# Kernel tuning notes

Hardware: AMD Instinct MI355X
Metric: run time of the kernel (lower is better)

## Reference

```python
import jax, jax.numpy as jnp
import numpy as np
import math

B, C, H, W = 8, 256, 64, 64
KEYDIM, VALDIM = 128, 256


def conv3x3(x, w, b):
    # x: [B,C,H,W], w: [O,C,3,3] -> [B,O,H,W], SAME padding (padding=1)
    y = jax.lax.conv_general_dilated(x, w, window_strides=(1, 1), padding='SAME',
                                     dimension_numbers=('NCHW', 'OIHW', 'NCHW'))
    return y + b[None, :, None, None]


def setup_inputs() -> dict:
    key = jax.random.key(0)
    ks = jax.random.split(key, 5)
    x = jax.random.normal(ks[0], (B, C, H, W), dtype=jnp.float32)
    fan_in = C * 9
    s = 1.0 / np.sqrt(fan_in)
    key_w = jax.random.uniform(ks[1], (KEYDIM, C, 3, 3), jnp.float32, -s, s)
    key_b = jax.random.uniform(ks[2], (KEYDIM,), jnp.float32, -s, s)
    val_w = jax.random.uniform(ks[3], (VALDIM, C, 3, 3), jnp.float32, -s, s)
    val_b = jax.random.uniform(ks[4], (VALDIM,), jnp.float32, -s, s)
    return {"x": x, "key_w": key_w, "key_b": key_b, "val_w": val_w, "val_b": val_b}


def reference(x, key_w, key_b, val_w, val_b):
    b_, c_, h_, w_ = x.shape
    k = conv3x3(x, key_w, key_b).reshape(b_, KEYDIM, h_ * w_)   # [B,K,N]
    v = conv3x3(x, val_w, val_b)                                 # [B,V,H,W]
    sq = jnp.sum(k * k, axis=1)                                  # [B,N]
    a = sq[:, :, None]                                           # [B,N,1]
    c2 = sq[:, None, :]                                          # [B,1,N]
    dots = 2.0 * jnp.einsum('bki,bkj->bij', k, k)                # [B,N,N]
    affinity = (-a + dots - c2) / math.sqrt(KEYDIM)              # -||ki-kj||^2 / sqrt(K)
    affinity = jax.nn.softmax(affinity, axis=1)                  # softmax over dim=1 (rows)
    self_attn = jnp.einsum('bvi,bij->bvj', v.reshape(b_, VALDIM, h_ * w_), affinity)
    self_attn = self_attn.reshape(b_, VALDIM, h_, w_)
    return jnp.concatenate((v, self_attn), axis=1)               # [B,2V,H,W]
```

## Files before the change

### kernel.cpp

```cpp
#include <hip/hip_runtime.h>
#include <hip/hip_bf16.h>
#include <cstdint>

constexpr int Bb = 8, Cc = 256, Hh = 64, Ww = 64, Nn = 4096;
constexpr int KD = 128, VD = 256, HP = 66;

typedef __attribute__((ext_vector_type(8))) short short8_t;
typedef __attribute__((ext_vector_type(4))) short shortx4;
typedef __attribute__((ext_vector_type(4))) float floatx4;

constexpr float kScale = 0.08838834764831845f * 1.4426950408889634f;
constexpr float kTwoK  = 2.0f * kScale;

static __device__ __forceinline__ ushort f2bf(float f) {
    union { float f; uint32_t u; } v{f};
    uint32_t r = v.u + 0x7FFFu + ((v.u >> 16) & 1u);
    return (ushort)(r >> 16);
}
static __device__ __forceinline__ float bf2f(ushort b) {
    union { uint32_t u; float f; } v{(uint32_t)b << 16};
    return v.f;
}
static __device__ __forceinline__ uint32_t pk_bf16(float a, float b) {
    uint32_t r;
    asm("v_cvt_pk_bf16_f32 %0, %1, %2" : "=v"(r) : "v"(a), "v"(b));
    return r;
}
static __device__ __forceinline__ float exp2_raw(float x) {
    float r;
    asm("v_exp_f32 %0, %1" : "=v"(r) : "v"(x));
    return r;
}

static __device__ __forceinline__ void gload_lds16(const void* g, void* l) {
    __builtin_amdgcn_global_load_lds((const __attribute__((address_space(1))) uint32_t*)g,
                                     (__attribute__((address_space(3))) uint32_t*)l, 16, 0, 0);
}

__global__ __launch_bounds__(256) void pad_transpose(const float* __restrict__ x,
                                                     ushort* __restrict__ xpad) {
    int bid = blockIdx.x;
    int b = bid & 7, rest = bid >> 3;
    int y = rest & 63, cg = rest >> 6;
    int t = threadIdx.x;
    __shared__ float tile[64][65];
    int xcol = t & 63;
    int crow = t >> 6;
    const float* xb = x + ((size_t)(b * Cc + cg * 64) * Nn) + y * 64;
#pragma unroll
    for (int i = 0; i < 16; i++) {
        int c = crow + i * 4;
        tile[c][xcol] = xb[(size_t)c * Nn + xcol];
    }
    __syncthreads();
    int c = t & 63;
    int x4 = t >> 6;
    ushort* dst = xpad + (((size_t)(b * HP + (y + 1)) * HP) + 1) * Cc + cg * 64 + c;
#pragma unroll
    for (int i = 0; i < 16; i++) {
        int xx = x4 + i * 4;
        dst[(size_t)xx * Cc] = f2bf(tile[c][xx]);
    }
}

__global__ __launch_bounds__(256) void repack_w(const float* __restrict__ kw,
                                                const float* __restrict__ vw,
                                                ushort* __restrict__ wtk,
                                                ushort* __restrict__ wtv) {
    int idx = blockIdx.x * 256 + threadIdx.x;
    const int nk = KD * Cc;
    const int nv = VD * Cc;
    if (idx < nk) {
        const float* src = kw + (size_t)idx * 9;
        int oc = idx / Cc, c = idx % Cc;
#pragma unroll
        for (int r = 0; r < 9; r++) wtk[((size_t)r * KD + oc) * Cc + c] = f2bf(src[r]);
    } else if (idx < nk + nv) {
        int j = idx - nk;
        const float* src = vw + (size_t)j * 9;
        int oc = j / Cc, c = j % Cc;
#pragma unroll
        for (int r = 0; r < 9; r++) wtv[((size_t)r * VD + oc) * Cc + c] = f2bf(src[r]);
    }
}

__global__ __launch_bounds__(256) void conv_k(const ushort* __restrict__ xpad,
                                              const ushort* __restrict__ wt,
                                              const float* __restrict__ bias,
                                              ushort* __restrict__ kt_out,
                                              float* __restrict__ sq_out) {
    int bid = blockIdx.x;
    int b = bid & 7, y = bid >> 3;
    int lane = threadIdx.x & 63, wv = threadIdx.x >> 6;
    int l15 = lane & 15, g = lane >> 4;
    const int swzA = l15 & 7;

    __shared__ ushort wslab[2][128 * 128];

    size_t wsoff[8];
    int ldsrow[8];
#pragma unroll
    for (int h = 0; h < 8; h++) {
        int row = wv * 32 + h * 4 + (lane >> 4);
        wsoff[h] = (size_t)row * Cc + (((lane & 15) ^ (row & 7)) * 8);
        ldsrow[h] = (wv * 32 + h * 4) * 128;
    }

    floatx4 acc[8];
#pragma unroll
    for (int m = 0; m < 8; m++) acc[m] = (floatx4){0.f, 0.f, 0.f, 0.f};

    const ushort* xb = xpad + ((size_t)b * HP * HP) * Cc;
    int xcol = wv * 16 + l15;

    auto stage = [&](int hs, int bi) {
        int r = hs >> 1, hc = hs & 1;
        const ushort* wb = wt + ((size_t)r * KD) * Cc + hc * 128;
#pragma unroll
        for (int h = 0; h < 8; h++)
            gload_lds16(wb + wsoff[h], &wslab[bi][ldsrow[h]]);
    };

    stage(0, 0);
    __syncthreads();

#pragma unroll 1
    for (int hs = 0; hs < 18; ++hs) {
        int bi = hs & 1;
        if (hs < 17) stage(hs + 1, bi ^ 1);

        int r = hs >> 1, hc = hs & 1;
        int dy = r / 3, dx = r % 3;
        const ushort* bsrc = xb + ((size_t)(y + dy) * HP + xcol + dx) * Cc + hc * 128 + g * 8;
#pragma unroll
        for (int cc = 0; cc < 4; cc++) {
            short8_t bfrag = *(const short8_t*)(bsrc + cc * 32);
#pragma unroll
            for (int m = 0; m < 8; m++) {
                short8_t afrag = *(const short8_t*)&wslab[bi][(m * 16 + l15) * 128 + ((cc * 4 + g) ^ swzA) * 8];
                acc[m] = __builtin_amdgcn_mfma_f32_16x16x32_bf16(afrag, bfrag, acc[m], 0, 0, 0);
            }
        }
        __syncthreads();
    }

    int pos = y * 64 + xcol;
    ushort* kt = kt_out + ((size_t)(b * Nn + pos)) * KD;
    float ssum = 0.f;
#pragma unroll
    for (int m = 0; m < 8; m++) {
        floatx4 bv = *(const floatx4*)(bias + m * 16 + g * 4);
        shortx4 pk;
#pragma unroll
        for (int r = 0; r < 4; r++) {
            pk[r] = (short)f2bf(acc[m][r] + bv[r]);
            float q = bf2f((ushort)pk[r]);
            ssum += q * q;
        }
        *(shortx4*)(kt + m * 16 + g * 4) = pk;
    }
    ssum += __shfl_xor(ssum, 16, 64);
    ssum += __shfl_xor(ssum, 32, 64);
    if (g == 0) sq_out[b * Nn + pos] = ssum * kScale;
}

__global__ __launch_bounds__(256) void conv_v(const ushort* __restrict__ xpad,
                                              const ushort* __restrict__ wt,
                                              const float* __restrict__ bias,
                                              float* __restrict__ f32_out,
                                              ushort* __restrict__ vb_out) {
    int bid = blockIdx.x;
    int b = bid & 7;
    int ocg = (bid >> 3) & 1;
    int y0 = (bid >> 4) * 2;
    int lane = threadIdx.x & 63, wv = threadIdx.x >> 6;
    int l15 = lane & 15, g = lane >> 4;
    int oc0 = ocg * 128;
    const int swzA = l15 & 7;

    __shared__ ushort wslab[2][128 * 128];

    size_t wsoff[8];
    int ldsrow[8];
#pragma unroll
    for (int h = 0; h < 8; h++) {
        int row = wv * 32 + h * 4 + (lane >> 4);
        wsoff[h] = (size_t)row * Cc + (((lane & 15) ^ (row & 7)) * 8);
        ldsrow[h] = (wv * 32 + h * 4) * 128;
    }

    floatx4 acc[8][2];
#pragma unroll
    for (int m = 0; m < 8; m++)
#pragma unroll
        for (int rr = 0; rr < 2; rr++) acc[m][rr] = (floatx4){0.f, 0.f, 0.f, 0.f};

    const ushort* xb = xpad + ((size_t)b * HP * HP) * Cc;
    int xcol = wv * 16 + l15;

    auto stage = [&](int hs, int bi) {
        int r = hs >> 1, hc = hs & 1;
        const ushort* wb = wt + ((size_t)r * VD + oc0) * Cc + hc * 128;
#pragma unroll
        for (int h = 0; h < 8; h++)
            gload_lds16(wb + wsoff[h], &wslab[bi][ldsrow[h]]);
    };

    stage(0, 0);
    __syncthreads();

#pragma unroll 1
    for (int hs = 0; hs < 18; ++hs) {
        int bi = hs & 1;
        if (hs < 17) stage(hs + 1, bi ^ 1);

        int r = hs >> 1, hc = hs & 1;
        int dy = r / 3, dx = r % 3;
        const ushort* bsrc0 = xb + ((size_t)(y0 + dy) * HP + xcol + dx) * Cc + hc * 128 + g * 8;
        const ushort* bsrc1 = bsrc0 + (size_t)HP * Cc;
#pragma unroll
        for (int cc = 0; cc < 4; cc++) {
            short8_t bfragA = *(const short8_t*)(bsrc0 + cc * 32);
            short8_t bfragB = *(const short8_t*)(bsrc1 + cc * 32);
#pragma unroll
            for (int m = 0; m < 8; m++) {
                short8_t afrag = *(const short8_t*)&wslab[bi][(m * 16 + l15) * 128 + ((cc * 4 + g) ^ swzA) * 8];
                acc[m][0] = __builtin_amdgcn_mfma_f32_16x16x32_bf16(afrag, bfragA, acc[m][0], 0, 0, 0);
                acc[m][1] = __builtin_amdgcn_mfma_f32_16x16x32_bf16(afrag, bfragB, acc[m][1], 0, 0, 0);
            }
        }
        __syncthreads();
    }

#pragma unroll
    for (int rr = 0; rr < 2; rr++) {
        int pos = (y0 + rr) * 64 + xcol;
#pragma unroll
        for (int m = 0; m < 8; m++) {
            floatx4 bv = *(const floatx4*)(bias + oc0 + m * 16 + g * 4);
#pragma unroll
            for (int r = 0; r < 4; r++) {
                int oc = oc0 + m * 16 + g * 4 + r;
                float v = acc[m][rr][r] + bv[r];
                f32_out[((size_t)(b * 512 + oc)) * Nn + pos] = v;
                vb_out[((size_t)(b * VD + oc)) * Nn + pos] = f2bf(v);
            }
        }
    }
}

__global__ __launch_bounds__(256) void attn_kernel(const ushort* __restrict__ kt,
                                                   const ushort* __restrict__ vb,
                                                   const float* __restrict__ sq2,
                                                   float* __restrict__ out) {
    int bid = blockIdx.x;
    int b = bid & 7, jt = bid >> 3;
    int lane = threadIdx.x & 63, wv = threadIdx.x >> 6;
    int l15 = lane & 15, g = lane >> 4;

    __shared__ ushort bufK[64 * 128];
    __shared__ ushort bufV[256 * 64];
    __shared__ ushort pt[4][16][72];
    __shared__ float dls[4][16];

    const ushort* ktb = kt + ((size_t)b * Nn) * KD;
    const ushort* vbb = vb + ((size_t)b * VD) * Nn;
    const float* sqb = sq2 + b * Nn;

    const ushort* skp[4];
#pragma unroll
    for (int h = 0; h < 4; h++) {
        int row = wv * 16 + h * 4 + (lane >> 4);
        skp[h] = ktb + (size_t)row * KD + (((lane & 15) ^ (row & 7)) * 8);
    }
    const ushort* svp[8];
#pragma unroll
    for (int h = 0; h < 8; h++) {
        int vd = wv * 64 + h * 8 + (lane >> 3);
        svp[h] = vbb + (size_t)vd * Nn + (((lane & 7) ^ (vd & 7)) * 8);
    }

    int j = jt * 64 + wv * 16 + l15;
    short8_t kj[4];
#pragma unroll
    for (int kk = 0; kk < 4; kk++)
        kj[kk] = *(const short8_t*)(ktb + (size_t)j * KD + kk * 32 + g * 8);

    const int vh = wv >> 1, jh = wv & 1;

    floatx4 acc[8][2];
#pragma unroll
    for (int m = 0; m < 8; m++)
#pragma unroll
        for (int s = 0; s < 2; s++) acc[m][s] = (floatx4){0.f, 0.f, 0.f, 0.f};
    float dsum = 0.f;
    const int swzA = l15 & 7;

#pragma unroll
    for (int h = 0; h < 4; h++) gload_lds16(skp[h], &bufK[(wv * 16 + h * 4) * 128]);
#pragma unroll
    for (int h = 0; h < 8; h++) gload_lds16(svp[h], &bufV[(wv * 64 + h * 8) * 64]);
    __syncthreads();

#pragma unroll 1
    for (int it = 0; it < 64; ++it) {
        int i0 = it * 64;

        floatx4 sacc[4];
#pragma unroll
        for (int f = 0; f < 4; f++) sacc[f] = (floatx4){0.f, 0.f, 0.f, 0.f};
#pragma unroll
        for (int kk = 0; kk < 4; kk++) {
#pragma unroll
            for (int f = 0; f < 4; f++) {
                short8_t afr = *(const short8_t*)&bufK[(f * 16 + l15) * 128 + ((kk * 4 + g) ^ swzA) * 8];
                sacc[f] = __builtin_amdgcn_mfma_f32_16x16x32_bf16(afr, kj[kk], sacc[f], 0, 0, 0);
            }
        }
#pragma unroll
        for (int f = 0; f < 4; f++) {
            floatx4 sqi = *(const floatx4*)(sqb + i0 + f * 16 + g * 4);
            float p0 = exp2_raw(sacc[f][0] * kTwoK - sqi[0]);
            float p1 = exp2_raw(sacc[f][1] * kTwoK - sqi[1]);
            float p2 = exp2_raw(sacc[f][2] * kTwoK - sqi[2]);
            float p3 = exp2_raw(sacc[f][3] * kTwoK - sqi[3]);
            dsum += (p0 + p1) + (p2 + p3);
            uint2 w2 = {pk_bf16(p0, p1), pk_bf16(p2, p3)};
            *(uint2*)&pt[wv][l15][f * 16 + g * 4] = w2;
        }
        __syncthreads();

        if (it < 63) {
#pragma unroll
            for (int h = 0; h < 4; h++)
                gload_lds16(skp[h] + (size_t)(i0 + 64) * KD, &bufK[(wv * 16 + h * 4) * 128]);
        }

#pragma unroll
        for (int k2 = 0; k2 < 2; k2++) {
            short8_t pfr[2];
#pragma unroll
            for (int s = 0; s < 2; s++)
                pfr[s] = *(const short8_t*)&pt[jh * 2 + s][l15][k2 * 32 + g * 8];
#pragma unroll
            for (int m = 0; m < 8; m++) {
                int row = vh * 128 + m * 16 + l15;
                short8_t vfr = *(const short8_t*)&bufV[row * 64 + ((k2 * 4 + g) ^ swzA) * 8];
#pragma unroll
                for (int s = 0; s < 2; s++)
                    acc[m][s] = __builtin_amdgcn_mfma_f32_16x16x32_bf16(vfr, pfr[s], acc[m][s], 0, 0, 0);
            }
        }
        __syncthreads();

        if (it < 63) {
#pragma unroll
            for (int h = 0; h < 8; h++)
                gload_lds16(svp[h] + (i0 + 64), &bufV[(wv * 64 + h * 8) * 64]);
        }
    }

    dsum += __shfl_xor(dsum, 16, 64);
    dsum += __shfl_xor(dsum, 32, 64);
    if (g == 0) dls[wv][l15] = dsum;
    __syncthreads();
    float rden[2];
#pragma unroll
    for (int s = 0; s < 2; s++) rden[s] = 1.f / dls[jh * 2 + s][l15];

    float* ob = out + ((size_t)(b * 512 + 256 + vh * 128)) * Nn + jt * 64 + jh * 32 + l15;
#pragma unroll
    for (int m = 0; m < 8; m++) {
#pragma unroll
        for (int s = 0; s < 2; s++) {
#pragma unroll
            for (int r = 0; r < 4; r++) {
                int vd = m * 16 + g * 4 + r;
                ob[(size_t)vd * Nn + s * 16] = acc[m][s][r] * rden[s];
            }
        }
    }
}

extern "C" void kernel_launch(void* const* d_in, const int* in_sizes, int n_in,
                              void* d_out, int out_size, void* d_ws, size_t ws_size,
                              hipStream_t stream) {
    const float* x     = (const float*)d_in[0];
    const float* kw    = (const float*)d_in[1];
    const float* kbias = (const float*)d_in[2];
    const float* vw    = (const float*)d_in[3];
    const float* vbias = (const float*)d_in[4];
    float* out = (float*)d_out;
    char* ws = (char*)d_ws;

    constexpr size_t XPAD = 0;
    constexpr size_t WTK  = 17842176;
    constexpr size_t WTV  = 18432000;
    constexpr size_t KT   = 19611648;
    constexpr size_t VB   = 28000256;
    constexpr size_t SQ   = 44777472;

    ushort* xpad = (ushort*)(ws + XPAD);
    ushort* wtk  = (ushort*)(ws + WTK);
    ushort* wtv  = (ushort*)(ws + WTV);
    ushort* ktw  = (ushort*)(ws + KT);
    ushort* vbw  = (ushort*)(ws + VB);
    float*  sqw  = (float*)(ws + SQ);

    hipMemsetAsync(xpad, 0, 17842176, stream);
    pad_transpose<<<dim3(2048), 256, 0, stream>>>(x, xpad);
    repack_w<<<dim3(384), 256, 0, stream>>>(kw, vw, wtk, wtv);
    conv_k<<<dim3(512), 256, 0, stream>>>(xpad, wtk, kbias, ktw, sqw);
    conv_v<<<dim3(512), 256, 0, stream>>>(xpad, wtv, vbias, out, vbw);
    attn_kernel<<<dim3(512), 256, 0, stream>>>(ktw, vbw, sqw, out);
}
```

Baseline: 247.5 us.

## Keep softmax probabilities in registers by permuting key rows, dropping LDS staging

The attention kernel now loads K rows into LDS in a permuted order, so each wave's S-tile accumulator layout matches the B-operand fragment layout of the PV MFMA. The probabilities are packed directly from registers into the second matmul's operand, which removes the pt LDS buffer and the dls cross-wave reduction. Each wave now owns its 16 output columns across all 256 value rows, instead of splitting V rows and columns across waves. The K prefetch is moved earlier, just after the QK MFMAs, and launch bounds request 3 blocks per SM. In exchange each wave holds 16 accumulator tiles and reads all of bufV, which raises register pressure and LDS read traffic per wave.

```diff
diff --git a/kernel.cpp b/kernel.cpp
--- a/kernel.cpp
+++ b/kernel.cpp
@@ -249,10 +249,10 @@
     }
 }
 
-__global__ __launch_bounds__(256) void attn_kernel(const ushort* __restrict__ kt,
-                                                   const ushort* __restrict__ vb,
-                                                   const float* __restrict__ sq2,
-                                                   float* __restrict__ out) {
+__global__ __launch_bounds__(256, 3) void attn_kernel(const ushort* __restrict__ kt,
+                                                      const ushort* __restrict__ vb,
+                                                      const float* __restrict__ sq2,
+                                                      float* __restrict__ out) {
     int bid = blockIdx.x;
     int b = bid & 7, jt = bid >> 3;
     int lane = threadIdx.x & 63, wv = threadIdx.x >> 6;
@@ -260,8 +260,6 @@
 
     __shared__ ushort bufK[64 * 128];
     __shared__ ushort bufV[256 * 64];
-    __shared__ ushort pt[4][16][72];
-    __shared__ float dls[4][16];
 
     const ushort* ktb = kt + ((size_t)b * Nn) * KD;
     const ushort* vbb = vb + ((size_t)b * VD) * Nn;
@@ -270,8 +268,10 @@
     const ushort* skp[4];
 #pragma unroll
     for (int h = 0; h < 4; h++) {
-        int row = wv * 16 + h * 4 + (lane >> 4);
-        skp[h] = ktb + (size_t)row * KD + (((lane & 15) ^ (row & 7)) * 8);
+        int sub = lane >> 4;
+        int pr = h * 4 + sub;
+        int ilog = ((wv & 1) << 5) + (h << 3) + ((wv >> 1) << 2) + sub;
+        skp[h] = ktb + (size_t)ilog * KD + ((l15 ^ (pr & 7)) * 8);
     }
     const ushort* svp[8];
 #pragma unroll
@@ -286,13 +286,9 @@
     for (int kk = 0; kk < 4; kk++)
         kj[kk] = *(const short8_t*)(ktb + (size_t)j * KD + kk * 32 + g * 8);
 
-    const int vh = wv >> 1, jh = wv & 1;
-
-    floatx4 acc[8][2];
-#pragma unroll
-    for (int m = 0; m < 8; m++)
-#pragma unroll
-        for (int s = 0; s < 2; s++) acc[m][s] = (floatx4){0.f, 0.f, 0.f, 0.f};
+    floatx4 acc[16];
+#pragma unroll
+    for (int m = 0; m < 16; m++) acc[m] = (floatx4){0.f, 0.f, 0.f, 0.f};
     float dsum = 0.f;
     const int swzA = l15 & 7;
 
@@ -317,38 +313,39 @@
                 sacc[f] = __builtin_amdgcn_mfma_f32_16x16x32_bf16(afr, kj[kk], sacc[f], 0, 0, 0);
             }
         }
+        __syncthreads();
+
+        if (it < 63) {
+#pragma unroll
+            for (int h = 0; h < 4; h++)
+                gload_lds16(skp[h] + (size_t)(i0 + 64) * KD, &bufK[(wv * 16 + h * 4) * 128]);
+        }
+
+        uint32_t w2[4][2];
 #pragma unroll
         for (int f = 0; f < 4; f++) {
-            floatx4 sqi = *(const floatx4*)(sqb + i0 + f * 16 + g * 4);
+            floatx4 sqi = *(const floatx4*)(sqb + i0 + ((f & 1) << 5) + (g << 3) + ((f >> 1) << 2));
             float p0 = exp2_raw(sacc[f][0] * kTwoK - sqi[0]);
             float p1 = exp2_raw(sacc[f][1] * kTwoK - sqi[1]);
             float p2 = exp2_raw(sacc[f][2] * kTwoK - sqi[2]);
             float p3 = exp2_raw(sacc[f][3] * kTwoK - sqi[3]);
             dsum += (p0 + p1) + (p2 + p3);
-            uint2 w2 = {pk_bf16(p0, p1), pk_bf16(p2, p3)};
-            *(uint2*)&pt[wv][l15][f * 16 + g * 4] = w2;
-        }
-        __syncthreads();
-
-        if (it < 63) {
-#pragma unroll
-            for (int h = 0; h < 4; h++)
-                gload_lds16(skp[h] + (size_t)(i0 + 64) * KD, &bufK[(wv * 16 + h * 4) * 128]);
+            w2[f][0] = pk_bf16(p0, p1);
+            w2[f][1] = pk_bf16(p2, p3);
         }
 
 #pragma unroll
         for (int k2 = 0; k2 < 2; k2++) {
-            short8_t pfr[2];
-#pragma unroll
-            for (int s = 0; s < 2; s++)
-                pfr[s] = *(const short8_t*)&pt[jh * 2 + s][l15][k2 * 32 + g * 8];
-#pragma unroll
-            for (int m = 0; m < 8; m++) {
-                int row = vh * 128 + m * 16 + l15;
-                short8_t vfr = *(const short8_t*)&bufV[row * 64 + ((k2 * 4 + g) ^ swzA) * 8];
-#pragma unroll
-                for (int s = 0; s < 2; s++)
-                    acc[m][s] = __builtin_amdgcn_mfma_f32_16x16x32_bf16(vfr, pfr[s], acc[m][s], 0, 0, 0);
+            union { uint32_t u[4]; short8_t s; } pu;
+            pu.u[0] = w2[k2][0];
+            pu.u[1] = w2[k2][1];
+            pu.u[2] = w2[k2 | 2][0];
+            pu.u[3] = w2[k2 | 2][1];
+            short8_t pfr = pu.s;
+#pragma unroll
+            for (int m = 0; m < 16; m++) {
+                short8_t vfr = *(const short8_t*)&bufV[(m * 16 + l15) * 64 + ((k2 * 4 + g) ^ swzA) * 8];
+                acc[m] = __builtin_amdgcn_mfma_f32_16x16x32_bf16(vfr, pfr, acc[m], 0, 0, 0);
             }
         }
         __syncthreads();
@@ -362,22 +359,15 @@
 
     dsum += __shfl_xor(dsum, 16, 64);
     dsum += __shfl_xor(dsum, 32, 64);
-    if (g == 0) dls[wv][l15] = dsum;
-    __syncthreads();
-    float rden[2];
-#pragma unroll
-    for (int s = 0; s < 2; s++) rden[s] = 1.f / dls[jh * 2 + s][l15];
-
-    float* ob = out + ((size_t)(b * 512 + 256 + vh * 128)) * Nn + jt * 64 + jh * 32 + l15;
-#pragma unroll
-    for (int m = 0; m < 8; m++) {
-#pragma unroll
-        for (int s = 0; s < 2; s++) {
-#pragma unroll
-            for (int r = 0; r < 4; r++) {
-                int vd = m * 16 + g * 4 + r;
-                ob[(size_t)vd * Nn + s * 16] = acc[m][s][r] * rden[s];
-            }
+    float rden = 1.f / dsum;
+
+    float* ob = out + ((size_t)(b * 512 + 256)) * Nn + j;
+#pragma unroll
+    for (int m = 0; m < 16; m++) {
+#pragma unroll
+        for (int r = 0; r < 4; r++) {
+            int vd = m * 16 + g * 4 + r;
+            ob[(size_t)vd * Nn] = acc[m][r] * rden;
         }
     }
 }
```

New measurement: 258.0 us. 1.04x slower.

## Keep softmax probabilities in registers by permuting K rows, drop LDS staging

Applied to the files above, without the earlier changes.

Each wave now computes the score tile for both 16-column j-slices it later consumes, instead of one slice shared through LDS. K rows are loaded into LDS in a permuted order, so each lane's MFMA score outputs line up with the B-operand layout of the PV MFMA and the bf16 probabilities are packed directly from registers. This removes the pt LDS buffer, its writes and reads, and the final LDS reduction barrier. In exchange the QK MFMA work is duplicated across the two waves sharing a j-half, register pressure rises, and a launch-bounds occupancy hint of 2 blocks per CU is added.

```diff
diff --git a/kernel.cpp b/kernel.cpp
--- a/kernel.cpp
+++ b/kernel.cpp
@@ -249,10 +249,10 @@
     }
 }
 
-__global__ __launch_bounds__(256) void attn_kernel(const ushort* __restrict__ kt,
-                                                   const ushort* __restrict__ vb,
-                                                   const float* __restrict__ sq2,
-                                                   float* __restrict__ out) {
+__global__ __launch_bounds__(256, 2) void attn_kernel(const ushort* __restrict__ kt,
+                                                      const ushort* __restrict__ vb,
+                                                      const float* __restrict__ sq2,
+                                                      float* __restrict__ out) {
     int bid = blockIdx.x;
     int b = bid & 7, jt = bid >> 3;
     int lane = threadIdx.x & 63, wv = threadIdx.x >> 6;
@@ -260,8 +260,6 @@
 
     __shared__ ushort bufK[64 * 128];
     __shared__ ushort bufV[256 * 64];
-    __shared__ ushort pt[4][16][72];
-    __shared__ float dls[4][16];
 
     const ushort* ktb = kt + ((size_t)b * Nn) * KD;
     const ushort* vbb = vb + ((size_t)b * VD) * Nn;
@@ -270,8 +268,10 @@
     const ushort* skp[4];
 #pragma unroll
     for (int h = 0; h < 4; h++) {
-        int row = wv * 16 + h * 4 + (lane >> 4);
-        skp[h] = ktb + (size_t)row * KD + (((lane & 15) ^ (row & 7)) * 8);
+        int sub = lane >> 4;
+        int pr = h * 4 + sub;
+        int ilog = ((wv & 1) << 5) + (h << 3) + ((wv >> 1) << 2) + sub;
+        skp[h] = ktb + (size_t)ilog * KD + ((l15 ^ (pr & 7)) * 8);
     }
     const ushort* svp[8];
 #pragma unroll
@@ -280,20 +280,23 @@
         svp[h] = vbb + (size_t)vd * Nn + (((lane & 7) ^ (vd & 7)) * 8);
     }
 
-    int j = jt * 64 + wv * 16 + l15;
-    short8_t kj[4];
-#pragma unroll
-    for (int kk = 0; kk < 4; kk++)
-        kj[kk] = *(const short8_t*)(ktb + (size_t)j * KD + kk * 32 + g * 8);
-
-    const int vh = wv >> 1, jh = wv & 1;
+    const int jh = wv & 1, vh = wv >> 1;
+
+    short8_t kj[2][4];
+#pragma unroll
+    for (int s = 0; s < 2; s++) {
+        int j = jt * 64 + jh * 32 + s * 16 + l15;
+#pragma unroll
+        for (int kk = 0; kk < 4; kk++)
+            kj[s][kk] = *(const short8_t*)(ktb + (size_t)j * KD + kk * 32 + g * 8);
+    }
 
     floatx4 acc[8][2];
 #pragma unroll
     for (int m = 0; m < 8; m++)
 #pragma unroll
         for (int s = 0; s < 2; s++) acc[m][s] = (floatx4){0.f, 0.f, 0.f, 0.f};
-    float dsum = 0.f;
+    float dsumv[2] = {0.f, 0.f};
     const int swzA = l15 & 7;
 
 #pragma unroll
@@ -306,27 +309,20 @@
     for (int it = 0; it < 64; ++it) {
         int i0 = it * 64;
 
-        floatx4 sacc[4];
-#pragma unroll
-        for (int f = 0; f < 4; f++) sacc[f] = (floatx4){0.f, 0.f, 0.f, 0.f};
+        floatx4 sacc[4][2];
+#pragma unroll
+        for (int f = 0; f < 4; f++)
+#pragma unroll
+            for (int s = 0; s < 2; s++) sacc[f][s] = (floatx4){0.f, 0.f, 0.f, 0.f};
 #pragma unroll
         for (int kk = 0; kk < 4; kk++) {
 #pragma unroll
             for (int f = 0; f < 4; f++) {
                 short8_t afr = *(const short8_t*)&bufK[(f * 16 + l15) * 128 + ((kk * 4 + g) ^ swzA) * 8];
-                sacc[f] = __builtin_amdgcn_mfma_f32_16x16x32_bf16(afr, kj[kk], sacc[f], 0, 0, 0);
-            }
-        }
-#pragma unroll
-        for (int f = 0; f < 4; f++) {
-            floatx4 sqi = *(const floatx4*)(sqb + i0 + f * 16 + g * 4);
-            float p0 = exp2_raw(sacc[f][0] * kTwoK - sqi[0]);
-            float p1 = exp2_raw(sacc[f][1] * kTwoK - sqi[1]);
-            float p2 = exp2_raw(sacc[f][2] * kTwoK - sqi[2]);
-            float p3 = exp2_raw(sacc[f][3] * kTwoK - sqi[3]);
-            dsum += (p0 + p1) + (p2 + p3);
-            uint2 w2 = {pk_bf16(p0, p1), pk_bf16(p2, p3)};
-            *(uint2*)&pt[wv][l15][f * 16 + g * 4] = w2;
+#pragma unroll
+                for (int s = 0; s < 2; s++)
+                    sacc[f][s] = __builtin_amdgcn_mfma_f32_16x16x32_bf16(afr, kj[s][kk], sacc[f][s], 0, 0, 0);
+            }
         }
         __syncthreads();
 
@@ -336,12 +332,34 @@
                 gload_lds16(skp[h] + (size_t)(i0 + 64) * KD, &bufK[(wv * 16 + h * 4) * 128]);
         }
 
+        uint32_t w2[4][2][2];
+#pragma unroll
+        for (int f = 0; f < 4; f++) {
+            floatx4 sqi = *(const floatx4*)(sqb + i0 + ((f & 1) << 5) + (g << 3) + ((f >> 1) << 2));
+#pragma unroll
+            for (int s = 0; s < 2; s++) {
+                float p0 = exp2_raw(sacc[f][s][0] * kTwoK - sqi[0]);
+                float p1 = exp2_raw(sacc[f][s][1] * kTwoK - sqi[1]);
+                float p2 = exp2_raw(sacc[f][s][2] * kTwoK - sqi[2]);
+                float p3 = exp2_raw(sacc[f][s][3] * kTwoK - sqi[3]);
+                dsumv[s] += (p0 + p1) + (p2 + p3);
+                w2[f][0][s] = pk_bf16(p0, p1);
+                w2[f][1][s] = pk_bf16(p2, p3);
+            }
+        }
+
 #pragma unroll
         for (int k2 = 0; k2 < 2; k2++) {
             short8_t pfr[2];
 #pragma unroll
-            for (int s = 0; s < 2; s++)
-                pfr[s] = *(const short8_t*)&pt[jh * 2 + s][l15][k2 * 32 + g * 8];
+            for (int s = 0; s < 2; s++) {
+                union { uint32_t u[4]; short8_t sv; } pu;
+                pu.u[0] = w2[k2][0][s];
+                pu.u[1] = w2[k2][1][s];
+                pu.u[2] = w2[k2 | 2][0][s];
+                pu.u[3] = w2[k2 | 2][1][s];
+                pfr[s] = pu.sv;
+            }
 #pragma unroll
             for (int m = 0; m < 8; m++) {
                 int row = vh * 128 + m * 16 + l15;
@@ -360,13 +378,12 @@
         }
     }
 
-    dsum += __shfl_xor(dsum, 16, 64);
-    dsum += __shfl_xor(dsum, 32, 64);
-    if (g == 0) dls[wv][l15] = dsum;
-    __syncthreads();
-    float rden[2];
-#pragma unroll
-    for (int s = 0; s < 2; s++) rden[s] = 1.f / dls[jh * 2 + s][l15];
+#pragma unroll
+    for (int s = 0; s < 2; s++) {
+        dsumv[s] += __shfl_xor(dsumv[s], 16, 64);
+        dsumv[s] += __shfl_xor(dsumv[s], 32, 64);
+    }
+    float rden[2] = {1.f / dsumv[0], 1.f / dsumv[1]};
 
     float* ob = out + ((size_t)(b * 512 + 256 + vh * 128)) * Nn + jt * 64 + jh * 32 + l15;
 #pragma unroll
```

New measurement: 270.7 us. 1.09x slower.
